# Performance work log

Hardware: AMD Instinct MI355X
Metric: run time of the kernel (lower is better)

The kernel has to match this reference:

```python
import jax, jax.numpy as jnp
import numpy as np

B, NPG, FANOUT = 32, 1024, 4       # graphs, nodes per graph, tree fan-out
H = 128                            # x_size == h_size
NUM_LAYERS = 4
A, BCAPS = 8, 8                    # TreeCaps a, b
DCC, N_CLASSES = 16, 50
ROUTING_ITER = 3
TYPE_VOCAB, TOKEN_VOCAB = 1000, 30000
EPS = 1e-10


def _build_forest():
    # parent of node i (i>0) is (i-1)//FANOUT; node 0 is root. Same tree per graph.
    child = np.arange(1, NPG)
    parent = (child - 1) // FANOUT
    pos = ((child - 1) % FANOUT).astype(np.float32)           # position in parent's mailbox
    cnt = np.bincount(parent, minlength=NPG).astype(np.float32)
    k = cnt[parent]                                           # child count of each edge's parent
    denom = np.maximum(k - 1.0, 1.0)
    lw = np.where(k == 1.0, 1.0, (k - 1.0 - pos) / denom).astype(np.float32)
    rw = np.where(k == 1.0, 0.0, pos / denom).astype(np.float32)
    offs = (np.arange(B) * NPG)[:, None]
    src = (child[None, :] + offs).reshape(-1).astype(np.int32)
    dst = (parent[None, :] + offs).reshape(-1).astype(np.int32)
    return src, dst, np.tile(lw, B), np.tile(rw, B), np.tile(cnt > 0, B)


def setup_inputs() -> dict:
    key = jax.random.key(0)
    ks = jax.random.split(key, 9)
    src, dst, lw, rw, has_children = _build_forest()
    N = B * NPG
    u = lambda k, s: jax.random.uniform(k, s, jnp.float32, -0.1, 0.1)
    return {
        "type_ids": jax.random.randint(ks[0], (N,), 0, TYPE_VOCAB, dtype=jnp.int32),
        "token_ids": jax.random.randint(ks[1], (N,), 0, TOKEN_VOCAB, dtype=jnp.int32),
        "src": jnp.asarray(src), "dst": jnp.asarray(dst),
        "lw": jnp.asarray(lw), "rw": jnp.asarray(rw),
        "has_children": jnp.asarray(has_children),
        "type_emb": jax.random.normal(ks[2], (TYPE_VOCAB, H - H // 2), jnp.float32),
        "token_emb": jax.random.normal(ks[3], (TOKEN_VOCAB, H // 2), jnp.float32),
        "W_left": u(ks[4], (NUM_LAYERS, H, H)),
        "W_right": u(ks[5], (NUM_LAYERS, H, H)),
        "W_top": u(ks[6], (NUM_LAYERS, H, H)),
        "b_conv": u(ks[7], (NUM_LAYERS, H)),
        "Wjm": 0.01 * jax.random.normal(ks[8], (A * H, DCC, N_CLASSES, NUM_LAYERS), jnp.float32),
    }


def squash(x, axis=-1):
    sq = jnp.sum(x * x, axis=axis, keepdims=True)
    return x * (sq / (1.0 + sq) / (jnp.sqrt(sq + EPS) + 1e-8))


def _vts_routing(uu):
    # uu: [NPG, H, L]  (one graph's primary capsules)
    l2 = jnp.sum(uu.reshape(NPG, -1) ** 2, axis=1)
    _, top_b = jax.lax.top_k(l2, BCAPS)
    u_i = jax.lax.stop_gradient(uu[top_b].reshape(-1, NUM_LAYERS))  # [BCAPS*H, L]
    _, top_a = jax.lax.top_k(l2, A)
    v_j = uu[top_a].reshape(-1, NUM_LAYERS)                         # [A*H, L]
    alpha = jnp.zeros((BCAPS * H, A * H), uu.dtype)
    for _ in range(ROUTING_ITER):
        alpha = alpha + u_i @ v_j.T
        beta = jax.nn.softmax(alpha, axis=-1)
        v_j = beta.T @ u_i
    return squash(v_j)                                              # [A*H, L]


def _dynamic_routing(SC, Wjm):
    # SC: [B, A*H, L], Wjm: [A*H, DCC, S, L]
    v = jnp.einsum('ncsm,bnm->bnsc', Wjm, SC)
    v_stop = jax.lax.stop_gradient(v)
    delta = jnp.zeros(SC.shape[:2] + (N_CLASSES,), SC.dtype)
    z = None
    for r in range(ROUTING_ITER):
        gamma = jax.nn.softmax(delta, axis=-1)
        vv = v if r == ROUTING_ITER - 1 else v_stop
        z = squash(jnp.einsum('bns,bnsc->bsc', gamma, vv))
        if r < ROUTING_ITER - 1:
            delta = delta + jnp.einsum('bnsc,bsc->bns', v_stop, z)
    return z                                                        # [B, S, DCC]


def reference(type_ids, token_ids, src, dst, lw, rw, has_children,
              type_emb, token_emb, W_left, W_right, W_top, b_conv, Wjm):
    h = jnp.concatenate([type_emb[type_ids], token_emb[token_ids]], axis=1)  # [N, H]
    N = h.shape[0]
    feats = []
    for l in range(NUM_LAYERS):
        ch = h[src]                                                 # [E, H] gather children
        msg = (ch @ W_left[l]) * lw[:, None] + (ch @ W_right[l]) * rw[:, None]
        children = jax.ops.segment_sum(msg, dst, num_segments=N)
        new_h = jax.nn.relu(children + h @ W_top[l] + b_conv[l][None, :])
        h = jnp.where(has_children[:, None], new_h, h)              # leaves keep old h
        feats.append(h)
    layer_feats = jnp.stack(feats, axis=-1)                         # [N, H, L]
    SC = jax.vmap(_vts_routing)(layer_feats.reshape(B, NPG, H, NUM_LAYERS))
    z = _dynamic_routing(SC, Wjm)
    logit = jnp.sqrt(jnp.sum(z * z, axis=-1) + EPS)                 # [B, S]
    return (logit, logit)
```

## Files before the change

### kernel.cpp

```cpp
#include <hip/hip_runtime.h>


#define BG      32
#define NPG     1024
#define HH      128
#define NLAY    4
#define INT_PG  256
#define M_INT   8192
#define NN      32768
#define EPG     1023
#define DCC     16
#define NS      50

__global__ void k_embed(const int* __restrict__ tids, const int* __restrict__ kids,
                        const float* __restrict__ temb, const float* __restrict__ kemb,
                        float* __restrict__ hA, float* __restrict__ hB) {
  int idx = blockIdx.x * 256 + threadIdx.x;
  int n = idx >> 5, c4 = idx & 31;
  float4 v;
  if (c4 < 16) v = *(const float4*)(temb + tids[n] * 64 + c4 * 4);
  else         v = *(const float4*)(kemb + kids[n] * 64 + (c4 - 16) * 4);
  *(float4*)(hA + n * 128 + c4 * 4) = v;
  if ((n & 1023) >= INT_PG)
    *(float4*)(hB + n * 128 + c4 * 4) = v;
}

__global__ __launch_bounds__(256) void k_conv(
    const float* __restrict__ hp, float* __restrict__ hn,
    const int* __restrict__ src, const float* __restrict__ lw,
    const float* __restrict__ rw,
    const float* __restrict__ Wl, const float* __restrict__ Wr,
    const float* __restrict__ Wt, const float* __restrict__ bias,
    float* __restrict__ feat) {
  __shared__ float Ws[32][128];
  __shared__ float AsT[32][40];
  __shared__ float hlS[32][128];
  __shared__ float hrS[32][128];
  int tid = threadIdx.x;
  int tx = tid & 31, ty = tid >> 5;
  int rowBase = blockIdx.x * 32;
  int g = rowBase >> 8, plBase = rowBase & 255;
  int nodeBase = g * NPG + plBase;

  #pragma unroll
  for (int t = 0; t < 4; ++t) {
    int it = tid + t * 256;
    int pw = it >> 5, c4 = it & 31;
    int pl = plBase + pw;
    float4 al = make_float4(0.f, 0.f, 0.f, 0.f);
    float4 ar = make_float4(0.f, 0.f, 0.f, 0.f);
    #pragma unroll
    for (int j = 0; j < 4; ++j) {
      int cc = 4 * pl + 1 + j;
      if (cc < NPG) {
        int e = g * EPG + cc - 1;
        int child = src[e];
        float lv = lw[e], rv = rw[e];
        float4 hv = *(const float4*)(hp + child * 128 + c4 * 4);
        al.x = fmaf(lv, hv.x, al.x); al.y = fmaf(lv, hv.y, al.y);
        al.z = fmaf(lv, hv.z, al.z); al.w = fmaf(lv, hv.w, al.w);
        ar.x = fmaf(rv, hv.x, ar.x); ar.y = fmaf(rv, hv.y, ar.y);
        ar.z = fmaf(rv, hv.z, ar.z); ar.w = fmaf(rv, hv.w, ar.w);
      }
    }
    *(float4*)&hlS[pw][c4 * 4] = al;
    *(float4*)&hrS[pw][c4 * 4] = ar;
  }
  __syncthreads();

  float acc[4][4] = {};
  int sr = tid >> 3, sc4 = (tid & 7) * 4;

  for (int kc = 0; kc < 12; ++kc) {
    int ssel = kc >> 2, kcol = (kc & 3) * 32;
    float4 av;
    if (ssel == 0)      av = *(const float4*)&hlS[sr][kcol + sc4];
    else if (ssel == 1) av = *(const float4*)&hrS[sr][kcol + sc4];
    else                av = *(const float4*)(hp + (nodeBase + sr) * 128 + kcol + sc4);
    const float* wsrc = ((ssel == 0) ? Wl : (ssel == 1) ? Wr : Wt) + kcol * 128;
    float4 wv0, wv1, wv2, wv3;
    {
      int f0 = tid, f1 = tid + 256, f2 = tid + 512, f3 = tid + 768;
      wv0 = *(const float4*)(wsrc + (f0 >> 5) * 128 + (f0 & 31) * 4);
      wv1 = *(const float4*)(wsrc + (f1 >> 5) * 128 + (f1 & 31) * 4);
      wv2 = *(const float4*)(wsrc + (f2 >> 5) * 128 + (f2 & 31) * 4);
      wv3 = *(const float4*)(wsrc + (f3 >> 5) * 128 + (f3 & 31) * 4);
    }
    __syncthreads();
    AsT[sc4 + 0][sr] = av.x; AsT[sc4 + 1][sr] = av.y;
    AsT[sc4 + 2][sr] = av.z; AsT[sc4 + 3][sr] = av.w;
    {
      int f0 = tid, f1 = tid + 256, f2 = tid + 512, f3 = tid + 768;
      *(float4*)&Ws[f0 >> 5][(f0 & 31) * 4] = wv0;
      *(float4*)&Ws[f1 >> 5][(f1 & 31) * 4] = wv1;
      *(float4*)&Ws[f2 >> 5][(f2 & 31) * 4] = wv2;
      *(float4*)&Ws[f3 >> 5][(f3 & 31) * 4] = wv3;
    }
    __syncthreads();
    #pragma unroll
    for (int kk = 0; kk < 32; ++kk) {
      float4 wv = *(float4*)&Ws[kk][tx * 4];
      float4 av2 = *(float4*)&AsT[kk][ty * 4];
      float aa[4] = {av2.x, av2.y, av2.z, av2.w};
      float ww[4] = {wv.x, wv.y, wv.z, wv.w};
      #pragma unroll
      for (int i = 0; i < 4; ++i)
        #pragma unroll
        for (int j = 0; j < 4; ++j)
          acc[i][j] = fmaf(aa[i], ww[j], acc[i][j]);
    }
  }
  float4 bv = *(const float4*)(bias + tx * 4);
  float bb[4] = {bv.x, bv.y, bv.z, bv.w};
  #pragma unroll
  for (int i = 0; i < 4; ++i) {
    int r = ty * 4 + i;
    float4 o = make_float4(fmaxf(acc[i][0] + bb[0], 0.f),
                           fmaxf(acc[i][1] + bb[1], 0.f),
                           fmaxf(acc[i][2] + bb[2], 0.f),
                           fmaxf(acc[i][3] + bb[3], 0.f));
    *(float4*)(feat + (rowBase + r) * 128 + tx * 4) = o;
    *(float4*)(hn + (nodeBase + r) * 128 + tx * 4) = o;
  }
}

__global__ void k_l2(const float* __restrict__ h, const float* __restrict__ feat,
                     float* __restrict__ l2) {
  int wid = (blockIdx.x * 256 + threadIdx.x) >> 6;
  int lane = threadIdx.x & 63;
  int g = wid >> 10, local = wid & 1023;
  float s = 0.f;
  if (local >= INT_PG) {
    const float* p = h + wid * 128;
    float a = p[lane], b = p[lane + 64];
    s = (a * a + b * b) * 4.f;
  } else {
    int row = (g * INT_PG + local) * 128;
    #pragma unroll
    for (int l = 0; l < 4; ++l) {
      const float* p = feat + l * (M_INT * 128) + row;
      float a = p[lane], b = p[lane + 64];
      s += a * a + b * b;
    }
  }
  #pragma unroll
  for (int off = 32; off; off >>= 1) s += __shfl_down(s, off);
  if (lane == 0) l2[wid] = s;
}

__global__ __launch_bounds__(256) void k_topk(const float* __restrict__ l2,
                                              int* __restrict__ sel) {
  int w = threadIdx.x >> 6, lane = threadIdx.x & 63;
  int g = blockIdx.x * 4 + w;
  unsigned long long kk[16];
  #pragma unroll
  for (int k = 0; k < 16; ++k) {
    int i = k * 64 + lane;
    unsigned vb = __float_as_uint(l2[g * 1024 + i]);
    kk[k] = ((unsigned long long)vb << 32) | (unsigned)(~i);
  }
  for (int r = 0; r < 8; ++r) {
    unsigned long long best = 0ULL;
    #pragma unroll
    for (int k = 0; k < 16; ++k) best = (kk[k] > best) ? kk[k] : best;
    #pragma unroll
    for (int off = 32; off; off >>= 1) {
      unsigned long long o = __shfl_down(best, off);
      best = (o > best) ? o : best;
    }
    best = __shfl(best, 0);
    if (lane == 0) sel[g * 8 + r] = (int)(~(unsigned)(best & 0xffffffffu));
    #pragma unroll
    for (int k = 0; k < 16; ++k) if (kk[k] == best) kk[k] = 0ULL;
  }
}

__global__ void k_buildU(const float* __restrict__ h, const float* __restrict__ feat,
                         const int* __restrict__ sel,
                         float* __restrict__ U, float* __restrict__ Vsum) {
  int idx = blockIdx.x * 256 + threadIdx.x;
  int g = idx >> 10, rank = (idx >> 7) & 7, hh = idx & 127;
  int local = sel[g * 8 + rank];
  float4 v;
  if (local >= INT_PG) {
    float x = h[(g * NPG + local) * 128 + hh];
    v = make_float4(x, x, x, x);
  } else {
    int row = (g * INT_PG + local) * 128 + hh;
    v.x = feat[row];
    v.y = feat[M_INT * 128 + row];
    v.z = feat[2 * M_INT * 128 + row];
    v.w = feat[3 * M_INT * 128 + row];
  }
  int o = g * 1024 + rank * 128 + hh;
  ((float4*)U)[o] = v;
  ((float4*)Vsum)[o] = v;
}

__global__ __launch_bounds__(1024) void k_vtsA(const float* __restrict__ U,
                                               const float* __restrict__ Vsum,
                                               float* __restrict__ mw, float* __restrict__ sw) {
  __shared__ float4 Vs[1024];
  __shared__ float2 red[1024];
  int g = blockIdx.x >> 3, rb = (blockIdx.x & 7) * 128;
  int tid = threadIdx.x, l = tid & 63, p = tid >> 6;
  Vs[tid] = ((const float4*)Vsum)[g * 1024 + tid];
  __syncthreads();
  float4 u0 = ((const float4*)U)[g * 1024 + rb + l];
  float4 u1 = ((const float4*)U)[g * 1024 + rb + 64 + l];
  int j0 = p * 64;
  float m0 = -3.4e38f, m1 = -3.4e38f;
  for (int j = j0; j < j0 + 64; ++j) {
    float4 v = Vs[j];
    float a0 = u0.x * v.x + u0.y * v.y + u0.z * v.z + u0.w * v.w;
    float a1 = u1.x * v.x + u1.y * v.y + u1.z * v.z + u1.w * v.w;
    m0 = fmaxf(m0, a0); m1 = fmaxf(m1, a1);
  }
  red[tid] = make_float2(m0, m1);
  __syncthreads();
  #pragma unroll
  for (int st = 512; st >= 64; st >>= 1) {
    if (tid < st) {
      float2 a = red[tid], b = red[tid + st];
      red[tid] = make_float2(fmaxf(a.x, b.x), fmaxf(a.y, b.y));
    }
    __syncthreads();
  }
  float2 mm = red[l];
  __syncthreads();
  float s0 = 0.f, s1 = 0.f;
  for (int j = j0; j < j0 + 64; ++j) {
    float4 v = Vs[j];
    float a0 = u0.x * v.x + u0.y * v.y + u0.z * v.z + u0.w * v.w;
    float a1 = u1.x * v.x + u1.y * v.y + u1.z * v.z + u1.w * v.w;
    s0 += __expf(a0 - mm.x);
    s1 += __expf(a1 - mm.y);
  }
  red[tid] = make_float2(s0, s1);
  __syncthreads();
  #pragma unroll
  for (int st = 512; st >= 64; st >>= 1) {
    if (tid < st) {
      float2 a = red[tid], b = red[tid + st];
      red[tid] = make_float2(a.x + b.x, a.y + b.y);
    }
    __syncthreads();
  }
  if (tid < 64) {
    float2 ss = red[tid];
    mw[g * 1024 + rb + tid] = mm.x;
    mw[g * 1024 + rb + 64 + tid] = mm.y;
    sw[g * 1024 + rb + tid] = ss.x;
    sw[g * 1024 + rb + 64 + tid] = ss.y;
  }
}

__global__ __launch_bounds__(1024) void k_vtsB(const float* __restrict__ U,
                                               float* __restrict__ Vsum,
                                               const float* __restrict__ mw,
                                               const float* __restrict__ sw,
                                               float* __restrict__ SCT, int last) {
  __shared__ float4 Us[1024];
  __shared__ float2 ms[1024];
  __shared__ float4 par[1024];
  int g = blockIdx.x >> 3, cb = (blockIdx.x & 7) * 128;
  int tid = threadIdx.x, l = tid & 63, p = tid >> 6;
  Us[tid] = ((const float4*)U)[g * 1024 + tid];
  ms[tid] = make_float2(mw[g * 1024 + tid], 1.0f / sw[g * 1024 + tid]);
  __syncthreads();
  float4 v0 = ((const float4*)Vsum)[g * 1024 + cb + l];
  float4 v1 = ((const float4*)Vsum)[g * 1024 + cb + 64 + l];
  float4 acc0 = make_float4(0.f, 0.f, 0.f, 0.f);
  float4 acc1 = make_float4(0.f, 0.f, 0.f, 0.f);
  int i0 = p * 64;
  for (int i = i0; i < i0 + 64; ++i) {
    float4 uu = Us[i];
    float2 st = ms[i];
    float a0 = uu.x * v0.x + uu.y * v0.y + uu.z * v0.z + uu.w * v0.w;
    float a1 = uu.x * v1.x + uu.y * v1.y + uu.z * v1.z + uu.w * v1.w;
    float w0 = __expf(a0 - st.x) * st.y;
    float w1 = __expf(a1 - st.x) * st.y;
    acc0.x = fmaf(w0, uu.x, acc0.x); acc0.y = fmaf(w0, uu.y, acc0.y);
    acc0.z = fmaf(w0, uu.z, acc0.z); acc0.w = fmaf(w0, uu.w, acc0.w);
    acc1.x = fmaf(w1, uu.x, acc1.x); acc1.y = fmaf(w1, uu.y, acc1.y);
    acc1.z = fmaf(w1, uu.z, acc1.z); acc1.w = fmaf(w1, uu.w, acc1.w);
  }
  par[tid] = acc0;
  __syncthreads();
  #pragma unroll
  for (int st = 512; st >= 64; st >>= 1) {
    if (tid < st) {
      float4 a = par[tid], b = par[tid + st];
      par[tid] = make_float4(a.x + b.x, a.y + b.y, a.z + b.z, a.w + b.w);
    }
    __syncthreads();
  }
  float4 o0;
  if (tid < 64) o0 = par[tid];
  __syncthreads();
  par[tid] = acc1;
  __syncthreads();
  #pragma unroll
  for (int st = 512; st >= 64; st >>= 1) {
    if (tid < st) {
      float4 a = par[tid], b = par[tid + st];
      par[tid] = make_float4(a.x + b.x, a.y + b.y, a.z + b.z, a.w + b.w);
    }
    __syncthreads();
  }
  if (tid < 64) {
    float4 o1 = par[tid];
    int j0c = cb + tid, j1c = cb + 64 + tid;
    if (last) {
      float sq0 = o0.x * o0.x + o0.y * o0.y + o0.z * o0.z + o0.w * o0.w;
      float f0 = (sq0 / (1.f + sq0)) / (sqrtf(sq0 + 1e-10f) + 1e-8f);
      ((float4*)SCT)[j0c * 32 + g] = make_float4(o0.x * f0, o0.y * f0, o0.z * f0, o0.w * f0);
      float sq1 = o1.x * o1.x + o1.y * o1.y + o1.z * o1.z + o1.w * o1.w;
      float f1 = (sq1 / (1.f + sq1)) / (sqrtf(sq1 + 1e-10f) + 1e-8f);
      ((float4*)SCT)[j1c * 32 + g] = make_float4(o1.x * f1, o1.y * f1, o1.z * f1, o1.w * f1);
    } else {
      float4 w0 = ((const float4*)Vsum)[g * 1024 + j0c];
      float4 w1 = ((const float4*)Vsum)[g * 1024 + j1c];
      ((float4*)Vsum)[g * 1024 + j0c] = make_float4(w0.x + o0.x, w0.y + o0.y,
                                                    w0.z + o0.z, w0.w + o0.w);
      ((float4*)Vsum)[g * 1024 + j1c] = make_float4(w1.x + o1.x, w1.y + o1.y,
                                                    w1.z + o1.z, w1.w + o1.w);
    }
  }
}

__global__ void k_transW(const float* __restrict__ Wjm, float* __restrict__ WT) {
  __shared__ float w[3200];
  int n = blockIdx.x, tid = threadIdx.x;
  for (int i = tid; i < 3200; i += 256) w[i] = Wjm[n * 3200 + i];
  __syncthreads();
  for (int i = tid; i < 3200; i += 256) {
    int s = i >> 6, cm = i & 63;
    int cc = cm >> 2, m = cm & 3;
    WT[(s * 1024 + n) * 64 + cm] = w[(cc * NS + s) * 4 + m];
  }
}

__global__ void k_gamma(const float* __restrict__ delta, float* __restrict__ gT) {
  int idx = blockIdx.x * 256 + threadIdx.x;
  int b = idx & 31, n = idx >> 5;
  const float* dp = delta + n * 32 + b;
  float d[NS];
  float m = -3.4e38f;
  #pragma unroll
  for (int s = 0; s < NS; ++s) { d[s] = dp[s * 32768]; m = fmaxf(m, d[s]); }
  float sum = 0.f;
  #pragma unroll
  for (int s = 0; s < NS; ++s) { d[s] = __expf(d[s] - m); sum += d[s]; }
  float inv = 1.0f / sum;
  float* gp = gT + n * 32 + b;
  #pragma unroll
  for (int s = 0; s < NS; ++s) gp[s * 32768] = d[s] * inv;
}

__global__ __launch_bounds__(256) void k_zsweep(const float* __restrict__ WT,
                                                const float* __restrict__ SCT,
                                                const float* __restrict__ gT,
                                                float* __restrict__ accZ, int it0) {
  int sb = blockIdx.x >> 4, nb = blockIdx.x & 15;
  int tid = threadIdx.x;
  int b = tid & 31, ch = tid >> 5;
  int n0 = nb * 64;
  const float4* wt = (const float4*)WT + (sb * 1024 + n0) * 16;
  const float4* sct = (const float4*)SCT + n0 * 32 + b;
  const float* gp = gT + (sb * 1024 + n0) * 32 + b;
  float a0 = 0.f, a1 = 0.f;
  #pragma unroll 4
  for (int nn = 0; nn < 64; ++nn) {
    float4 w0 = wt[nn * 16 + ch];
    float4 w1 = wt[nn * 16 + ch + 8];
    float4 s4 = sct[nn * 32];
    float gm = it0 ? (1.0f / 50.0f) : gp[nn * 32];
    float t0 = w0.x * s4.x + w0.y * s4.y + w0.z * s4.z + w0.w * s4.w;
    float t1 = w1.x * s4.x + w1.y * s4.y + w1.z * s4.z + w1.w * s4.w;
    a0 = fmaf(gm, t0, a0);
    a1 = fmaf(gm, t1, a1);
  }
  atomicAdd(accZ + (b * NS + sb) * 16 + ch, a0);
  atomicAdd(accZ + (b * NS + sb) * 16 + ch + 8, a1);
}

__global__ void k_logits(const float* __restrict__ accZ, float* __restrict__ out) {
  int idx = blockIdx.x * 256 + threadIdx.x;
  if (idx >= 1600) return;
  const float4* a4 = (const float4*)accZ + idx * 4;
  float4 u0 = a4[0], u1 = a4[1], u2 = a4[2], u3 = a4[3];
  float sq = u0.x * u0.x + u0.y * u0.y + u0.z * u0.z + u0.w * u0.w
           + u1.x * u1.x + u1.y * u1.y + u1.z * u1.z + u1.w * u1.w
           + u2.x * u2.x + u2.y * u2.y + u2.z * u2.z + u2.w * u2.w
           + u3.x * u3.x + u3.y * u3.y + u3.z * u3.z + u3.w * u3.w;
  float f = (sq / (1.f + sq)) / (sqrtf(sq + 1e-10f) + 1e-8f);
  float lg = sqrtf(sq * f * f + 1e-10f);
  out[idx] = lg;
  out[idx + 1600] = lg;
}

__global__ __launch_bounds__(256) void k_dsweep(const float* __restrict__ WT,
                                                const float* __restrict__ SCT,
                                                const float* __restrict__ accZ,
                                                float* __restrict__ delta, int first) {
  __shared__ float wl[50 * 64];
  __shared__ float4 scl[32];
  int n = blockIdx.x;
  int tid = threadIdx.x;
  for (int i = tid; i < 3200; i += 256)
    wl[i] = WT[((i >> 6) * 1024 + n) * 64 + (i & 63)];
  if (tid < 32) scl[tid] = ((const float4*)SCT)[n * 32 + tid];
  __syncthreads();
  for (int idx = tid; idx < 1600; idx += 256) {
    int s = idx >> 5, b = idx & 31;
    const float4* wp = (const float4*)(wl + s * 64);
    const float4* zp = (const float4*)(accZ + (b * 50 + s) * 16);
    float4 u0 = zp[0], u1 = zp[1], u2 = zp[2], u3 = zp[3];
    float sq = u0.x * u0.x + u0.y * u0.y + u0.z * u0.z + u0.w * u0.w
             + u1.x * u1.x + u1.y * u1.y + u1.z * u1.z + u1.w * u1.w
             + u2.x * u2.x + u2.y * u2.y + u2.z * u2.z + u2.w * u2.w
             + u3.x * u3.x + u3.y * u3.y + u3.z * u3.z + u3.w * u3.w;
    float f = (sq / (1.f + sq)) / (sqrtf(sq + 1e-10f) + 1e-8f);
    float zs[16] = {u0.x * f, u0.y * f, u0.z * f, u0.w * f,
                    u1.x * f, u1.y * f, u1.z * f, u1.w * f,
                    u2.x * f, u2.y * f, u2.z * f, u2.w * f,
                    u3.x * f, u3.y * f, u3.z * f, u3.w * f};
    float4 y = make_float4(0.f, 0.f, 0.f, 0.f);
    #pragma unroll
    for (int c = 0; c < 16; ++c) {
      float4 w = wp[c];
      float zc = zs[c];
      y.x = fmaf(zc, w.x, y.x); y.y = fmaf(zc, w.y, y.y);
      y.z = fmaf(zc, w.z, y.z); y.w = fmaf(zc, w.w, y.w);
    }
    float4 sc = scl[b];
    float dd = sc.x * y.x + sc.y * y.y + sc.z * y.z + sc.w * y.w;
    float* dp = delta + (s * 1024 + n) * 32 + b;
    if (first) *dp = dd; else *dp = *dp + dd;
  }
}

extern "C" void kernel_launch(void* const* d_in, const int* in_sizes, int n_in,
                              void* d_out, int out_size, void* d_ws, size_t ws_size,
                              hipStream_t stream) {
  const int*   type_ids  = (const int*)d_in[0];
  const int*   token_ids = (const int*)d_in[1];
  const int*   src       = (const int*)d_in[2];
  const float* lw        = (const float*)d_in[4];
  const float* rw        = (const float*)d_in[5];
  const float* temb      = (const float*)d_in[7];
  const float* kemb      = (const float*)d_in[8];
  const float* Wl        = (const float*)d_in[9];
  const float* Wr        = (const float*)d_in[10];
  const float* Wt        = (const float*)d_in[11];
  const float* bconv     = (const float*)d_in[12];
  const float* Wjm       = (const float*)d_in[13];
  float* out = (float*)d_out;
  char* wsb = (char*)d_ws;

  float* hA    = (float*)(wsb + 0);
  float* hB    = (float*)(wsb + 16777216);
  float* feat  = (float*)(wsb + 33554432);
  float* WT    = (float*)(wsb + 50331648);
  float* delta = (float*)(wsb + 63963136);
  float* gT    = (float*)(wsb + 71303168);
  float* accZ  = (float*)(wsb + 78643200);
  float* l2b   = (float*)(wsb + 78774272);
  int*   sel   = (int*)  (wsb + 78905344);
  float* U     = (float*)(wsb + 78909440);
  float* Vsum  = (float*)(wsb + 79433728);
  float* mw    = (float*)(wsb + 79958016);
  float* sw    = (float*)(wsb + 80089088);
  float* SCT   = (float*)(wsb + 80220160);

  k_embed<<<4096, 256, 0, stream>>>(type_ids, token_ids, temb, kemb, hA, hB);
  k_transW<<<1024, 256, 0, stream>>>(Wjm, WT);

  for (int l = 0; l < NLAY; ++l) {
    const float* hp = (l & 1) ? hB : hA;
    float*       hn = (l & 1) ? hA : hB;
    k_conv<<<256, 256, 0, stream>>>(hp, hn, src, lw, rw,
                                    Wl + l * 16384, Wr + l * 16384, Wt + l * 16384,
                                    bconv + l * 128, feat + l * (M_INT * 128));
  }

  k_l2<<<8192, 256, 0, stream>>>(hA, feat, l2b);
  k_topk<<<8, 256, 0, stream>>>(l2b, sel);
  k_buildU<<<128, 256, 0, stream>>>(hA, feat, sel, U, Vsum);

  for (int it = 0; it < 3; ++it) {
    k_vtsA<<<256, 1024, 0, stream>>>(U, Vsum, mw, sw);
    k_vtsB<<<256, 1024, 0, stream>>>(U, Vsum, mw, sw, SCT, it == 2 ? 1 : 0);
  }

  for (int it = 0; it < 3; ++it) {
    if (it > 0) k_gamma<<<128, 256, 0, stream>>>(delta, gT);
    hipMemsetAsync(accZ, 0, 32 * 50 * 16 * 4, stream);
    k_zsweep<<<800, 256, 0, stream>>>(WT, SCT, gT, accZ, it == 0 ? 1 : 0);
    if (it < 2) k_dsweep<<<1024, 256, 0, stream>>>(WT, SCT, accZ, delta, it == 0 ? 1 : 0);
  }
  k_logits<<<7, 256, 0, stream>>>(accZ, out);
}
```

Before: 523.7 us.

## Split conv gather, halve tile sizes, fuse topk/buildU and gamma into dsweep

After: 476.3 us. 9.1% less time.

```diff
diff --git a/kernel.cpp b/kernel.cpp
--- a/kernel.cpp
+++ b/kernel.cpp
@@ -14,70 +14,63 @@
 
 __global__ void k_embed(const int* __restrict__ tids, const int* __restrict__ kids,
                         const float* __restrict__ temb, const float* __restrict__ kemb,
-                        float* __restrict__ hA, float* __restrict__ hB) {
+                        float* __restrict__ h) {
   int idx = blockIdx.x * 256 + threadIdx.x;
   int n = idx >> 5, c4 = idx & 31;
   float4 v;
   if (c4 < 16) v = *(const float4*)(temb + tids[n] * 64 + c4 * 4);
   else         v = *(const float4*)(kemb + kids[n] * 64 + (c4 - 16) * 4);
-  *(float4*)(hA + n * 128 + c4 * 4) = v;
-  if ((n & 1023) >= INT_PG)
-    *(float4*)(hB + n * 128 + c4 * 4) = v;
+  *(float4*)(h + n * 128 + c4 * 4) = v;
+}
+
+__global__ void k_gather(const float* __restrict__ h, const int* __restrict__ src,
+                         const float* __restrict__ lw, const float* __restrict__ rw,
+                         float* __restrict__ hl, float* __restrict__ hr) {
+  int idx = blockIdx.x * 256 + threadIdx.x;
+  int p = idx >> 5, c4 = idx & 31;
+  int g = p >> 8, pl = p & 255;
+  float4 al = make_float4(0.f, 0.f, 0.f, 0.f);
+  float4 ar = make_float4(0.f, 0.f, 0.f, 0.f);
+  for (int j = 0; j < 4; ++j) {
+    int cc = 4 * pl + 1 + j;
+    if (cc < NPG) {
+      int e = g * EPG + cc - 1;
+      int child = src[e];
+      float lv = lw[e], rv = rw[e];
+      float4 hv = *(const float4*)(h + child * 128 + c4 * 4);
+      al.x = fmaf(lv, hv.x, al.x); al.y = fmaf(lv, hv.y, al.y);
+      al.z = fmaf(lv, hv.z, al.z); al.w = fmaf(lv, hv.w, al.w);
+      ar.x = fmaf(rv, hv.x, ar.x); ar.y = fmaf(rv, hv.y, ar.y);
+      ar.z = fmaf(rv, hv.z, ar.z); ar.w = fmaf(rv, hv.w, ar.w);
+    }
+  }
+  *(float4*)(hl + p * 128 + c4 * 4) = al;
+  *(float4*)(hr + p * 128 + c4 * 4) = ar;
 }
 
 __global__ __launch_bounds__(256) void k_conv(
-    const float* __restrict__ hp, float* __restrict__ hn,
-    const int* __restrict__ src, const float* __restrict__ lw,
-    const float* __restrict__ rw,
+    const float* __restrict__ hl, const float* __restrict__ hr,
+    float* __restrict__ h,
     const float* __restrict__ Wl, const float* __restrict__ Wr,
     const float* __restrict__ Wt, const float* __restrict__ bias,
     float* __restrict__ feat) {
   __shared__ float Ws[32][128];
-  __shared__ float AsT[32][40];
-  __shared__ float hlS[32][128];
-  __shared__ float hrS[32][128];
+  __shared__ float AsT[32][20];
   int tid = threadIdx.x;
   int tx = tid & 31, ty = tid >> 5;
-  int rowBase = blockIdx.x * 32;
-  int g = rowBase >> 8, plBase = rowBase & 255;
-  int nodeBase = g * NPG + plBase;
-
-  #pragma unroll
-  for (int t = 0; t < 4; ++t) {
-    int it = tid + t * 256;
-    int pw = it >> 5, c4 = it & 31;
-    int pl = plBase + pw;
-    float4 al = make_float4(0.f, 0.f, 0.f, 0.f);
-    float4 ar = make_float4(0.f, 0.f, 0.f, 0.f);
-    #pragma unroll
-    for (int j = 0; j < 4; ++j) {
-      int cc = 4 * pl + 1 + j;
-      if (cc < NPG) {
-        int e = g * EPG + cc - 1;
-        int child = src[e];
-        float lv = lw[e], rv = rw[e];
-        float4 hv = *(const float4*)(hp + child * 128 + c4 * 4);
-        al.x = fmaf(lv, hv.x, al.x); al.y = fmaf(lv, hv.y, al.y);
-        al.z = fmaf(lv, hv.z, al.z); al.w = fmaf(lv, hv.w, al.w);
-        ar.x = fmaf(rv, hv.x, ar.x); ar.y = fmaf(rv, hv.y, ar.y);
-        ar.z = fmaf(rv, hv.z, ar.z); ar.w = fmaf(rv, hv.w, ar.w);
-      }
-    }
-    *(float4*)&hlS[pw][c4 * 4] = al;
-    *(float4*)&hrS[pw][c4 * 4] = ar;
-  }
-  __syncthreads();
-
-  float acc[4][4] = {};
+  int rowBase = blockIdx.x * 16;
+  int nodeBase = ((rowBase >> 8) << 10) + (rowBase & 255);
+  float acc[2][4] = {};
   int sr = tid >> 3, sc4 = (tid & 7) * 4;
 
   for (int kc = 0; kc < 12; ++kc) {
     int ssel = kc >> 2, kcol = (kc & 3) * 32;
-    float4 av;
-    if (ssel == 0)      av = *(const float4*)&hlS[sr][kcol + sc4];
-    else if (ssel == 1) av = *(const float4*)&hrS[sr][kcol + sc4];
-    else                av = *(const float4*)(hp + (nodeBase + sr) * 128 + kcol + sc4);
+    const float* ap = (ssel == 0) ? (hl + rowBase * 128)
+                    : (ssel == 1) ? (hr + rowBase * 128)
+                                  : (h + nodeBase * 128);
     const float* wsrc = ((ssel == 0) ? Wl : (ssel == 1) ? Wr : Wt) + kcol * 128;
+    float4 av = make_float4(0.f, 0.f, 0.f, 0.f);
+    if (tid < 128) av = *(const float4*)(ap + sr * 128 + kcol + sc4);
     float4 wv0, wv1, wv2, wv3;
     {
       int f0 = tid, f1 = tid + 256, f2 = tid + 512, f3 = tid + 768;
@@ -87,8 +80,10 @@
       wv3 = *(const float4*)(wsrc + (f3 >> 5) * 128 + (f3 & 31) * 4);
     }
     __syncthreads();
-    AsT[sc4 + 0][sr] = av.x; AsT[sc4 + 1][sr] = av.y;
-    AsT[sc4 + 2][sr] = av.z; AsT[sc4 + 3][sr] = av.w;
+    if (tid < 128) {
+      AsT[sc4 + 0][sr] = av.x; AsT[sc4 + 1][sr] = av.y;
+      AsT[sc4 + 2][sr] = av.z; AsT[sc4 + 3][sr] = av.w;
+    }
     {
       int f0 = tid, f1 = tid + 256, f2 = tid + 512, f3 = tid + 768;
       *(float4*)&Ws[f0 >> 5][(f0 & 31) * 4] = wv0;
@@ -100,11 +95,11 @@
     #pragma unroll
     for (int kk = 0; kk < 32; ++kk) {
       float4 wv = *(float4*)&Ws[kk][tx * 4];
-      float4 av2 = *(float4*)&AsT[kk][ty * 4];
-      float aa[4] = {av2.x, av2.y, av2.z, av2.w};
+      float2 av2 = *(float2*)&AsT[kk][ty * 2];
+      float aa[2] = {av2.x, av2.y};
       float ww[4] = {wv.x, wv.y, wv.z, wv.w};
       #pragma unroll
-      for (int i = 0; i < 4; ++i)
+      for (int i = 0; i < 2; ++i)
         #pragma unroll
         for (int j = 0; j < 4; ++j)
           acc[i][j] = fmaf(aa[i], ww[j], acc[i][j]);
@@ -113,14 +108,14 @@
   float4 bv = *(const float4*)(bias + tx * 4);
   float bb[4] = {bv.x, bv.y, bv.z, bv.w};
   #pragma unroll
-  for (int i = 0; i < 4; ++i) {
-    int r = ty * 4 + i;
+  for (int i = 0; i < 2; ++i) {
+    int r = ty * 2 + i;
     float4 o = make_float4(fmaxf(acc[i][0] + bb[0], 0.f),
                            fmaxf(acc[i][1] + bb[1], 0.f),
                            fmaxf(acc[i][2] + bb[2], 0.f),
                            fmaxf(acc[i][3] + bb[3], 0.f));
     *(float4*)(feat + (rowBase + r) * 128 + tx * 4) = o;
-    *(float4*)(hn + (nodeBase + r) * 128 + tx * 4) = o;
+    *(float4*)(h + (nodeBase + r) * 128 + tx * 4) = o;
   }
 }
 
@@ -148,110 +143,101 @@
   if (lane == 0) l2[wid] = s;
 }
 
-__global__ __launch_bounds__(256) void k_topk(const float* __restrict__ l2,
-                                              int* __restrict__ sel) {
-  int w = threadIdx.x >> 6, lane = threadIdx.x & 63;
-  int g = blockIdx.x * 4 + w;
-  unsigned long long kk[16];
-  #pragma unroll
-  for (int k = 0; k < 16; ++k) {
-    int i = k * 64 + lane;
-    unsigned vb = __float_as_uint(l2[g * 1024 + i]);
-    kk[k] = ((unsigned long long)vb << 32) | (unsigned)(~i);
-  }
-  for (int r = 0; r < 8; ++r) {
-    unsigned long long best = 0ULL;
+__global__ __launch_bounds__(256) void k_topsel(const float* __restrict__ l2,
+                                                const float* __restrict__ h,
+                                                const float* __restrict__ feat,
+                                                float* __restrict__ U,
+                                                float* __restrict__ Vsum) {
+  __shared__ int ssel[8];
+  int g = blockIdx.x, tid = threadIdx.x;
+  int lane = tid & 63;
+  if (tid < 64) {
+    unsigned long long kk[16];
     #pragma unroll
-    for (int k = 0; k < 16; ++k) best = (kk[k] > best) ? kk[k] : best;
-    #pragma unroll
-    for (int off = 32; off; off >>= 1) {
-      unsigned long long o = __shfl_down(best, off);
-      best = (o > best) ? o : best;
-    }
-    best = __shfl(best, 0);
-    if (lane == 0) sel[g * 8 + r] = (int)(~(unsigned)(best & 0xffffffffu));
-    #pragma unroll
-    for (int k = 0; k < 16; ++k) if (kk[k] == best) kk[k] = 0ULL;
-  }
-}
-
-__global__ void k_buildU(const float* __restrict__ h, const float* __restrict__ feat,
-                         const int* __restrict__ sel,
-                         float* __restrict__ U, float* __restrict__ Vsum) {
-  int idx = blockIdx.x * 256 + threadIdx.x;
-  int g = idx >> 10, rank = (idx >> 7) & 7, hh = idx & 127;
-  int local = sel[g * 8 + rank];
-  float4 v;
-  if (local >= INT_PG) {
-    float x = h[(g * NPG + local) * 128 + hh];
-    v = make_float4(x, x, x, x);
-  } else {
-    int row = (g * INT_PG + local) * 128 + hh;
-    v.x = feat[row];
-    v.y = feat[M_INT * 128 + row];
-    v.z = feat[2 * M_INT * 128 + row];
-    v.w = feat[3 * M_INT * 128 + row];
-  }
-  int o = g * 1024 + rank * 128 + hh;
-  ((float4*)U)[o] = v;
-  ((float4*)Vsum)[o] = v;
+    for (int k = 0; k < 16; ++k) {
+      int i = k * 64 + lane;
+      unsigned vb = __float_as_uint(l2[g * 1024 + i]);
+      kk[k] = ((unsigned long long)vb << 32) | (unsigned)(~i);
+    }
+    for (int r = 0; r < 8; ++r) {
+      unsigned long long best = 0ULL;
+      #pragma unroll
+      for (int k = 0; k < 16; ++k) best = (kk[k] > best) ? kk[k] : best;
+      #pragma unroll
+      for (int off = 32; off; off >>= 1) {
+        unsigned long long o = __shfl_down(best, off);
+        best = (o > best) ? o : best;
+      }
+      best = __shfl(best, 0);
+      if (lane == 0) ssel[r] = (int)(~(unsigned)(best & 0xffffffffu));
+      #pragma unroll
+      for (int k = 0; k < 16; ++k) if (kk[k] == best) kk[k] = 0ULL;
+    }
+  }
+  __syncthreads();
+  for (int t = 0; t < 4; ++t) {
+    int idx = t * 256 + tid;
+    int rank = idx >> 7, hh = idx & 127;
+    int local = ssel[rank];
+    float4 v;
+    if (local >= INT_PG) {
+      float x = h[(g * NPG + local) * 128 + hh];
+      v = make_float4(x, x, x, x);
+    } else {
+      int row = (g * INT_PG + local) * 128 + hh;
+      v.x = feat[row];
+      v.y = feat[M_INT * 128 + row];
+      v.z = feat[2 * M_INT * 128 + row];
+      v.w = feat[3 * M_INT * 128 + row];
+    }
+    int o = g * 1024 + rank * 128 + hh;
+    ((float4*)U)[o] = v;
+    ((float4*)Vsum)[o] = v;
+  }
 }
 
 __global__ __launch_bounds__(1024) void k_vtsA(const float* __restrict__ U,
                                                const float* __restrict__ Vsum,
                                                float* __restrict__ mw, float* __restrict__ sw) {
   __shared__ float4 Vs[1024];
-  __shared__ float2 red[1024];
-  int g = blockIdx.x >> 3, rb = (blockIdx.x & 7) * 128;
+  __shared__ float red[1024];
+  int g = blockIdx.x >> 4, rb = (blockIdx.x & 15) * 64;
   int tid = threadIdx.x, l = tid & 63, p = tid >> 6;
   Vs[tid] = ((const float4*)Vsum)[g * 1024 + tid];
   __syncthreads();
-  float4 u0 = ((const float4*)U)[g * 1024 + rb + l];
-  float4 u1 = ((const float4*)U)[g * 1024 + rb + 64 + l];
+  float4 u = ((const float4*)U)[g * 1024 + rb + l];
   int j0 = p * 64;
-  float m0 = -3.4e38f, m1 = -3.4e38f;
+  float m = -3.4e38f;
   for (int j = j0; j < j0 + 64; ++j) {
     float4 v = Vs[j];
-    float a0 = u0.x * v.x + u0.y * v.y + u0.z * v.z + u0.w * v.w;
-    float a1 = u1.x * v.x + u1.y * v.y + u1.z * v.z + u1.w * v.w;
-    m0 = fmaxf(m0, a0); m1 = fmaxf(m1, a1);
-  }
-  red[tid] = make_float2(m0, m1);
+    float a = u.x * v.x + u.y * v.y + u.z * v.z + u.w * v.w;
+    m = fmaxf(m, a);
+  }
+  red[tid] = m;
   __syncthreads();
   #pragma unroll
   for (int st = 512; st >= 64; st >>= 1) {
-    if (tid < st) {
-      float2 a = red[tid], b = red[tid + st];
-      red[tid] = make_float2(fmaxf(a.x, b.x), fmaxf(a.y, b.y));
-    }
+    if (tid < st) red[tid] = fmaxf(red[tid], red[tid + st]);
     __syncthreads();
   }
-  float2 mm = red[l];
-  __syncthreads();
-  float s0 = 0.f, s1 = 0.f;
+  float mm = red[l];
+  __syncthreads();
+  float s = 0.f;
   for (int j = j0; j < j0 + 64; ++j) {
     float4 v = Vs[j];
-    float a0 = u0.x * v.x + u0.y * v.y + u0.z * v.z + u0.w * v.w;
-    float a1 = u1.x * v.x + u1.y * v.y + u1.z * v.z + u1.w * v.w;
-    s0 += __expf(a0 - mm.x);
-    s1 += __expf(a1 - mm.y);
-  }
-  red[tid] = make_float2(s0, s1);
+    float a = u.x * v.x + u.y * v.y + u.z * v.z + u.w * v.w;
+    s += __expf(a - mm);
+  }
+  red[tid] = s;
   __syncthreads();
   #pragma unroll
   for (int st = 512; st >= 64; st >>= 1) {
-    if (tid < st) {
-      float2 a = red[tid], b = red[tid + st];
-      red[tid] = make_float2(a.x + b.x, a.y + b.y);
-    }
+    if (tid < st) red[tid] = red[tid] + red[tid + st];
     __syncthreads();
   }
   if (tid < 64) {
-    float2 ss = red[tid];
-    mw[g * 1024 + rb + tid] = mm.x;
-    mw[g * 1024 + rb + 64 + tid] = mm.y;
-    sw[g * 1024 + rb + tid] = ss.x;
-    sw[g * 1024 + rb + 64 + tid] = ss.y;
+    mw[g * 1024 + rb + tid] = mm;
+    sw[g * 1024 + rb + tid] = red[tid];
   }
 }
 
@@ -263,29 +249,23 @@
   __shared__ float4 Us[1024];
   __shared__ float2 ms[1024];
   __shared__ float4 par[1024];
-  int g = blockIdx.x >> 3, cb = (blockIdx.x & 7) * 128;
+  int g = blockIdx.x >> 4, cb = (blockIdx.x & 15) * 64;
   int tid = threadIdx.x, l = tid & 63, p = tid >> 6;
   Us[tid] = ((const float4*)U)[g * 1024 + tid];
   ms[tid] = make_float2(mw[g * 1024 + tid], 1.0f / sw[g * 1024 + tid]);
   __syncthreads();
-  float4 v0 = ((const float4*)Vsum)[g * 1024 + cb + l];
-  float4 v1 = ((const float4*)Vsum)[g * 1024 + cb + 64 + l];
-  float4 acc0 = make_float4(0.f, 0.f, 0.f, 0.f);
-  float4 acc1 = make_float4(0.f, 0.f, 0.f, 0.f);
+  float4 v = ((const float4*)Vsum)[g * 1024 + cb + l];
+  float4 acc = make_float4(0.f, 0.f, 0.f, 0.f);
   int i0 = p * 64;
   for (int i = i0; i < i0 + 64; ++i) {
     float4 uu = Us[i];
     float2 st = ms[i];
-    float a0 = uu.x * v0.x + uu.y * v0.y + uu.z * v0.z + uu.w * v0.w;
-    float a1 = uu.x * v1.x + uu.y * v1.y + uu.z * v1.z + uu.w * v1.w;
-    float w0 = __expf(a0 - st.x) * st.y;
-    float w1 = __expf(a1 - st.x) * st.y;
-    acc0.x = fmaf(w0, uu.x, acc0.x); acc0.y = fmaf(w0, uu.y, acc0.y);
-    acc0.z = fmaf(w0, uu.z, acc0.z); acc0.w = fmaf(w0, uu.w, acc0.w);
-    acc1.x = fmaf(w1, uu.x, acc1.x); acc1.y = fmaf(w1, uu.y, acc1.y);
-    acc1.z = fmaf(w1, uu.z, acc1.z); acc1.w = fmaf(w1, uu.w, acc1.w);
-  }
-  par[tid] = acc0;
+    float a = uu.x * v.x + uu.y * v.y + uu.z * v.z + uu.w * v.w;
+    float w = __expf(a - st.x) * st.y;
+    acc.x = fmaf(w, uu.x, acc.x); acc.y = fmaf(w, uu.y, acc.y);
+    acc.z = fmaf(w, uu.z, acc.z); acc.w = fmaf(w, uu.w, acc.w);
+  }
+  par[tid] = acc;
   __syncthreads();
   #pragma unroll
   for (int st = 512; st >= 64; st >>= 1) {
@@ -295,36 +275,17 @@
     }
     __syncthreads();
   }
-  float4 o0;
-  if (tid < 64) o0 = par[tid];
-  __syncthreads();
-  par[tid] = acc1;
-  __syncthreads();
-  #pragma unroll
-  for (int st = 512; st >= 64; st >>= 1) {
-    if (tid < st) {
-      float4 a = par[tid], b = par[tid + st];
-      par[tid] = make_float4(a.x + b.x, a.y + b.y, a.z + b.z, a.w + b.w);
-    }
-    __syncthreads();
-  }
   if (tid < 64) {
-    float4 o1 = par[tid];
-    int j0c = cb + tid, j1c = cb + 64 + tid;
+    float4 o = par[tid];
+    int jc = cb + tid;
     if (last) {
-      float sq0 = o0.x * o0.x + o0.y * o0.y + o0.z * o0.z + o0.w * o0.w;
-      float f0 = (sq0 / (1.f + sq0)) / (sqrtf(sq0 + 1e-10f) + 1e-8f);
-      ((float4*)SCT)[j0c * 32 + g] = make_float4(o0.x * f0, o0.y * f0, o0.z * f0, o0.w * f0);
-      float sq1 = o1.x * o1.x + o1.y * o1.y + o1.z * o1.z + o1.w * o1.w;
-      float f1 = (sq1 / (1.f + sq1)) / (sqrtf(sq1 + 1e-10f) + 1e-8f);
-      ((float4*)SCT)[j1c * 32 + g] = make_float4(o1.x * f1, o1.y * f1, o1.z * f1, o1.w * f1);
+      float sq = o.x * o.x + o.y * o.y + o.z * o.z + o.w * o.w;
+      float f = (sq / (1.f + sq)) / (sqrtf(sq + 1e-10f) + 1e-8f);
+      ((float4*)SCT)[jc * 32 + g] = make_float4(o.x * f, o.y * f, o.z * f, o.w * f);
     } else {
-      float4 w0 = ((const float4*)Vsum)[g * 1024 + j0c];
-      float4 w1 = ((const float4*)Vsum)[g * 1024 + j1c];
-      ((float4*)Vsum)[g * 1024 + j0c] = make_float4(w0.x + o0.x, w0.y + o0.y,
-                                                    w0.z + o0.z, w0.w + o0.w);
-      ((float4*)Vsum)[g * 1024 + j1c] = make_float4(w1.x + o1.x, w1.y + o1.y,
-                                                    w1.z + o1.z, w1.w + o1.w);
+      float4 w0 = ((const float4*)Vsum)[g * 1024 + jc];
+      ((float4*)Vsum)[g * 1024 + jc] = make_float4(w0.x + o.x, w0.y + o.y,
+                                                   w0.z + o.z, w0.w + o.w);
     }
   }
 }
@@ -339,23 +300,6 @@
     int cc = cm >> 2, m = cm & 3;
     WT[(s * 1024 + n) * 64 + cm] = w[(cc * NS + s) * 4 + m];
   }
-}
-
-__global__ void k_gamma(const float* __restrict__ delta, float* __restrict__ gT) {
-  int idx = blockIdx.x * 256 + threadIdx.x;
-  int b = idx & 31, n = idx >> 5;
-  const float* dp = delta + n * 32 + b;
-  float d[NS];
-  float m = -3.4e38f;
-  #pragma unroll
-  for (int s = 0; s < NS; ++s) { d[s] = dp[s * 32768]; m = fmaxf(m, d[s]); }
-  float sum = 0.f;
-  #pragma unroll
-  for (int s = 0; s < NS; ++s) { d[s] = __expf(d[s] - m); sum += d[s]; }
-  float inv = 1.0f / sum;
-  float* gp = gT + n * 32 + b;
-  #pragma unroll
-  for (int s = 0; s < NS; ++s) gp[s * 32768] = d[s] * inv;
 }
 
 __global__ __launch_bounds__(256) void k_zsweep(const float* __restrict__ WT,
@@ -403,9 +347,12 @@
 __global__ __launch_bounds__(256) void k_dsweep(const float* __restrict__ WT,
                                                 const float* __restrict__ SCT,
                                                 const float* __restrict__ accZ,
-                                                float* __restrict__ delta, int first) {
+                                                float* __restrict__ delta,
+                                                float* __restrict__ gT, int first) {
   __shared__ float wl[50 * 64];
   __shared__ float4 scl[32];
+  __shared__ float dtot[NS][32];
+  __shared__ float mb[32], ib[32];
   int n = blockIdx.x;
   int tid = threadIdx.x;
   for (int i = tid; i < 3200; i += 256)
@@ -436,8 +383,22 @@
     }
     float4 sc = scl[b];
     float dd = sc.x * y.x + sc.y * y.y + sc.z * y.z + sc.w * y.w;
-    float* dp = delta + (s * 1024 + n) * 32 + b;
-    if (first) *dp = dd; else *dp = *dp + dd;
+    float dt = first ? dd : (delta[(s * 1024 + n) * 32 + b] + dd);
+    dtot[s][b] = dt;
+    if (first) delta[(s * 1024 + n) * 32 + b] = dt;
+  }
+  __syncthreads();
+  if (tid < 32) {
+    float m = -3.4e38f;
+    for (int s = 0; s < NS; ++s) m = fmaxf(m, dtot[s][tid]);
+    float sum = 0.f;
+    for (int s = 0; s < NS; ++s) sum += __expf(dtot[s][tid] - m);
+    mb[tid] = m; ib[tid] = 1.0f / sum;
+  }
+  __syncthreads();
+  for (int idx = tid; idx < 1600; idx += 256) {
+    int s = idx >> 5, b = idx & 31;
+    gT[(s * 1024 + n) * 32 + b] = __expf(dtot[s][b] - mb[b]) * ib[b];
   }
 }
 
@@ -459,46 +420,45 @@
   float* out = (float*)d_out;
   char* wsb = (char*)d_ws;
 
-  float* hA    = (float*)(wsb + 0);
-  float* hB    = (float*)(wsb + 16777216);
-  float* feat  = (float*)(wsb + 33554432);
-  float* WT    = (float*)(wsb + 50331648);
-  float* delta = (float*)(wsb + 63963136);
-  float* gT    = (float*)(wsb + 71303168);
-  float* accZ  = (float*)(wsb + 78643200);
-  float* l2b   = (float*)(wsb + 78774272);
-  int*   sel   = (int*)  (wsb + 78905344);
-  float* U     = (float*)(wsb + 78909440);
-  float* Vsum  = (float*)(wsb + 79433728);
-  float* mw    = (float*)(wsb + 79958016);
-  float* sw    = (float*)(wsb + 80089088);
-  float* SCT   = (float*)(wsb + 80220160);
-
-  k_embed<<<4096, 256, 0, stream>>>(type_ids, token_ids, temb, kemb, hA, hB);
+  float* h     = (float*)(wsb + 0);
+  float* feat  = (float*)(wsb + 16777216);
+  float* WT    = (float*)(wsb + 33554432);
+  float* delta = (float*)(wsb + 46661632);
+  float* gT    = (float*)(wsb + 53215232);
+  float* accZ  = (float*)(wsb + 59768832);
+  float* l2b   = (float*)(wsb + 60076032);
+  float* U     = (float*)(wsb + 60207104);
+  float* Vsum  = (float*)(wsb + 60731392);
+  float* mw    = (float*)(wsb + 61255680);
+  float* sw    = (float*)(wsb + 61386752);
+  float* SCT   = (float*)(wsb + 61517824);
+  float* hl    = (float*)(wsb + 62042112);
+  float* hr    = (float*)(wsb + 66236416);
+
+  k_embed<<<4096, 256, 0, stream>>>(type_ids, token_ids, temb, kemb, h);
   k_transW<<<1024, 256, 0, stream>>>(Wjm, WT);
+  hipMemsetAsync(accZ, 0, 3 * 32 * 50 * 16 * 4, stream);
 
   for (int l = 0; l < NLAY; ++l) {
-    const float* hp = (l & 1) ? hB : hA;
-    float*       hn = (l & 1) ? hA : hB;
-    k_conv<<<256, 256, 0, stream>>>(hp, hn, src, lw, rw,
+    k_gather<<<1024, 256, 0, stream>>>(h, src, lw, rw, hl, hr);
+    k_conv<<<512, 256, 0, stream>>>(hl, hr, h,
                                     Wl + l * 16384, Wr + l * 16384, Wt + l * 16384,
                                     bconv + l * 128, feat + l * (M_INT * 128));
   }
 
-  k_l2<<<8192, 256, 0, stream>>>(hA, feat, l2b);
-  k_topk<<<8, 256, 0, stream>>>(l2b, sel);
-  k_buildU<<<128, 256, 0, stream>>>(hA, feat, sel, U, Vsum);
+  k_l2<<<8192, 256, 0, stream>>>(h, feat, l2b);
+  k_topsel<<<32, 256, 0, stream>>>(l2b, h, feat, U, Vsum);
 
   for (int it = 0; it < 3; ++it) {
-    k_vtsA<<<256, 1024, 0, stream>>>(U, Vsum, mw, sw);
-    k_vtsB<<<256, 1024, 0, stream>>>(U, Vsum, mw, sw, SCT, it == 2 ? 1 : 0);
+    k_vtsA<<<512, 1024, 0, stream>>>(U, Vsum, mw, sw);
+    k_vtsB<<<512, 1024, 0, stream>>>(U, Vsum, mw, sw, SCT, it == 2 ? 1 : 0);
   }
 
   for (int it = 0; it < 3; ++it) {
-    if (it > 0) k_gamma<<<128, 256, 0, stream>>>(delta, gT);
-    hipMemsetAsync(accZ, 0, 32 * 50 * 16 * 4, stream);
-    k_zsweep<<<800, 256, 0, stream>>>(WT, SCT, gT, accZ, it == 0 ? 1 : 0);
-    if (it < 2) k_dsweep<<<1024, 256, 0, stream>>>(WT, SCT, accZ, delta, it == 0 ? 1 : 0);
-  }
-  k_logits<<<7, 256, 0, stream>>>(accZ, out);
-}
+    float* aZ = accZ + it * 25600;
+    k_zsweep<<<800, 256, 0, stream>>>(WT, SCT, gT, aZ, it == 0 ? 1 : 0);
+    if (it < 2)
+      k_dsweep<<<1024, 256, 0, stream>>>(WT, SCT, aZ, delta, gT, it == 0 ? 1 : 0);
+  }
+  k_logits<<<7, 256, 0, stream>>>(accZ + 2 * 25600, out);
+}
```
